# Kernel tuning notes

Hardware: AMD Instinct MI355X
Metric: run time of the kernel (lower is better)

Reference implementation:

```python
import jax, jax.numpy as jnp
import numpy as np

B, A, G, C, P, PH, PW = 8, 19248, 32, 81, 32, 138, 138
K_POS = 128            # fixed upper bound on positives used for the mask loss
INPUT_SIZE = 550.0
POS_THR, NEG_THR = 0.5, 0.4
ALPHA, GAMMA = 0.25, 2.0
NEG_POS_RATIO = 3
CLS_W, BOX_W, MASK_W = 1.0, 1.5, 6.125
VAR_XY, VAR_WH = 0.1, 0.2
EPS = 1e-6


def setup_inputs() -> dict:
    key = jax.random.key(0)
    ks = jax.random.split(key, 10)
    class_preds = jax.random.normal(ks[0], (B, A, C), jnp.float32)
    box_preds = jax.random.normal(ks[1], (B, A, 4), jnp.float32) * 0.1
    mask_coeffs = jax.random.normal(ks[2], (B, A, P), jnp.float32)
    prototypes = jax.random.normal(ks[3], (B, P, PH, PW), jnp.float32)
    # anchors in normalized [cx, cy, w, h]
    cxy = jax.random.uniform(ks[4], (A, 2), jnp.float32)
    wh = jax.random.uniform(ks[5], (A, 2), jnp.float32) * 0.25 + 0.02
    anchors = jnp.concatenate([cxy, wh], axis=-1)
    # GT boxes in absolute pixels [x1, y1, x2, y2] within 550x550
    xy1 = jax.random.uniform(ks[6], (B, G, 2), jnp.float32) * 380.0
    bwh = jax.random.uniform(ks[7], (B, G, 2), jnp.float32) * 150.0 + 15.0
    gt_boxes = jnp.concatenate([xy1, xy1 + bwh], axis=-1)
    gt_labels = jax.random.randint(ks[8], (B, G), 1, C)  # foreground classes
    gt_masks = (jax.random.uniform(ks[9], (B, G, PH, PW)) > 0.5).astype(jnp.float32)
    return {
        "class_preds": class_preds, "box_preds": box_preds,
        "mask_coeffs": mask_coeffs, "prototypes": prototypes,
        "anchors": anchors, "gt_boxes": gt_boxes,
        "gt_labels": gt_labels, "gt_masks": gt_masks,
    }


def _iou(a, b):
    # a: (A,4) xyxy, b: (G,4) xyxy -> (A,G)
    max_xy = jnp.minimum(a[:, None, 2:], b[None, :, 2:])
    min_xy = jnp.maximum(a[:, None, :2], b[None, :, :2])
    inter = jnp.clip(max_xy - min_xy, 0.0).prod(-1)
    area_a = (a[:, 2] - a[:, 0]) * (a[:, 3] - a[:, 1])
    area_b = (b[:, 2] - b[:, 0]) * (b[:, 3] - b[:, 1])
    union = area_a[:, None] + area_b[None, :] - inter
    return inter / jnp.clip(union, EPS)


def _smooth_l1(x):
    d = jnp.abs(x)
    return jnp.where(d < 1.0, 0.5 * d * d, d - 0.5)


def _image_loss(cls_p, box_p, coeffs, protos, gtb, gtl, gtm, anchors, anchors_xyxy):
    gtb = gtb / INPUT_SIZE                           # normalize to [0,1]
    iou = _iou(anchors_xyxy, gtb)                    # (A, G)
    best_gt_iou = iou.max(axis=1)                    # (A,)
    best_gt_idx = iou.argmax(axis=1)                 # (A,)
    best_anchor_idx = iou.argmax(axis=0)             # (G,) bipartite guarantee

    pos = best_gt_iou >= POS_THR
    pos = pos.at[best_anchor_idx].set(True)
    best_gt_idx = best_gt_idx.at[best_anchor_idx].set(jnp.arange(G))
    neg = (best_gt_iou < NEG_THR) & ~pos
    num_pos = pos.sum()
    # deterministic hard-negative cap at neg:pos = 3:1 (orig. uses randperm)
    neg = neg & (jnp.cumsum(neg) <= num_pos * NEG_POS_RATIO)

    matched_labels = jnp.where(pos, gtl[best_gt_idx], 0)   # 0 = background
    mb = gtb[best_gt_idx]                                  # (A,4) matched xyxy
    posf = pos.astype(jnp.float32)

    # ---- focal classification loss over pos|neg anchors ----
    probs = jax.nn.softmax(cls_p, axis=-1)
    p_t = jnp.take_along_axis(probs, matched_labels[:, None], axis=1)[:, 0]
    p_t = jnp.clip(p_t, EPS, 1.0 - EPS)
    alpha_t = jnp.where(matched_labels > 0, ALPHA, 1.0 - ALPHA)
    focal = alpha_t * (1.0 - p_t) ** GAMMA * (-jnp.log(p_t))
    cls_loss = (focal * (pos | neg).astype(jnp.float32)).sum()

    acx, acy, aw, ah = anchors[:, 0], anchors[:, 1], anchors[:, 2], anchors[:, 3]
    gcx = 0.5 * (mb[:, 0] + mb[:, 2]); gcy = 0.5 * (mb[:, 1] + mb[:, 3])
    gw = jnp.clip(mb[:, 2] - mb[:, 0], EPS); gh = jnp.clip(mb[:, 3] - mb[:, 1], EPS)
    t = jnp.stack([
        (gcx - acx) / (aw * VAR_XY),
        (gcy - acy) / (ah * VAR_XY),
        jnp.log(gw / aw) / VAR_WH,
        jnp.log(gh / ah) / VAR_WH,
    ], axis=-1)                                            # (A,4)
    box_loss = (_smooth_l1(box_p - t).sum(-1) * posf).sum()

    # ---- BCE mask loss on (up to K_POS) positive anchors ----
    score = jnp.where(pos, best_gt_iou + 1.0, 0.0)
    _, idx = jax.lax.top_k(score, K_POS)                   # (K,)
    w = posf[idx]                                          # 0-weight padding
    logits = jnp.einsum('kp,phw->khw', coeffs[idx], protos)  # (K,PH,PW)
    tgt = gtm[best_gt_idx[idx]]                            # (K,PH,PW)
    bce = jnp.maximum(logits, 0.0) - logits * tgt + jnp.log1p(jnp.exp(-jnp.abs(logits)))
    mask_loss = (bce.mean(axis=(1, 2)) * w).sum()

    return cls_loss, box_loss, mask_loss, num_pos


def reference(class_preds, box_preds, mask_coeffs, prototypes, anchors, gt_boxes, gt_labels, gt_masks):
    a_xyxy = jnp.concatenate(
        [anchors[:, :2] - anchors[:, 2:] * 0.5, anchors[:, :2] + anchors[:, 2:] * 0.5], axis=-1)
    cls_l, box_l, mask_l, npos = jax.vmap(
        _image_loss, in_axes=(0, 0, 0, 0, 0, 0, 0, None, None)
    )(class_preds, box_preds, mask_coeffs, prototypes, gt_boxes, gt_labels, gt_masks, anchors, a_xyxy)
    denom = jnp.maximum(npos.sum(), 1).astype(jnp.float32)
    total = (CLS_W * cls_l.sum() + BOX_W * box_l.sum() + MASK_W * mask_l.sum()) / denom
    return total
```

## Files before the change

### kernel.cpp

```cpp
#include <hip/hip_runtime.h>
#include <math.h>

#define BB 8
#define AA 19248
#define GG 32
#define CC 81
#define PP 32
#define PHW 19044
#define KPOS 128
#define NEGRATIO 3
#define SELCAP 7680
#define NWCH 304
#define NB1 76
#define NB0 75
#define NPT 1191
#define NB7 298
#define NB45 8

typedef _Float16 half8 __attribute__((ext_vector_type(8)));
typedef float floatx4 __attribute__((ext_vector_type(4)));

__device__ __forceinline__ float iou_one(float ax1, float ay1, float ax2, float ay2,
                                         float areaA,
                                         float gx1, float gy1, float gx2, float gy2) {
#pragma clang fp contract(off)
    float ix1 = fmaxf(ax1, gx1), iy1 = fmaxf(ay1, gy1);
    float ix2 = fminf(ax2, gx2), iy2 = fminf(ay2, gy2);
    float iw = fmaxf(ix2 - ix1, 0.0f), ih = fmaxf(iy2 - iy1, 0.0f);
    float inter = iw * ih;
    float areaB = (gx2 - gx1) * (gy2 - gy1);
    float u = areaA + areaB - inter;
    u = fmaxf(u, 1e-6f);
    return inter / u;
}

__global__ __launch_bounds__(256) void k01(
    const float* __restrict__ anchors, const float* __restrict__ gt_boxes,
    const float* __restrict__ protos, const float* __restrict__ gtm,
    float* __restrict__ best_iou, int* __restrict__ best_g,
    unsigned long long* __restrict__ gkey_part, float* __restrict__ acc,
    _Float16* __restrict__ protoT, unsigned* __restrict__ pmask) {
#pragma clang fp contract(off)
    int b = blockIdx.y;
    __shared__ float sg[GG][4];
    __shared__ unsigned long long s_gk[GG];

    if (blockIdx.x >= NB1) {
        int px = (blockIdx.x - NB1) * 256 + threadIdx.x;
        if (px >= PHW) return;
        const float* pb = protos + (size_t)b * PP * PHW + px;
        _Float16 v[PP];
        #pragma unroll
        for (int k = 0; k < PP; ++k)
            v[k] = (_Float16)pb[(size_t)k * PHW];
        half8* dst = (half8*)&protoT[((size_t)b * PHW + px) * PP];
        #pragma unroll
        for (int q = 0; q < 4; ++q)
            dst[q] = *(half8*)&v[q * 8];
        const float* gb = gtm + (size_t)b * GG * PHW + px;
        unsigned m = 0u;
        #pragma unroll
        for (int g = 0; g < GG; ++g)
            m |= (gb[(size_t)g * PHW] > 0.5f) ? (1u << g) : 0u;
        pmask[(size_t)b * PHW + px] = m;
        return;
    }

    int a = blockIdx.x * 256 + threadIdx.x;
    int lane = threadIdx.x & 63;
    if (blockIdx.x == 0 && b == 0 && threadIdx.x < 4)
        ((int*)acc)[threadIdx.x] = 0;
    for (int t = threadIdx.x; t < GG * 4; t += 256)
        sg[t >> 2][t & 3] = gt_boxes[b * GG * 4 + t] / 550.0f;
    if (threadIdx.x < GG) s_gk[threadIdx.x] = 0ULL;
    __syncthreads();
    bool valid = a < AA;
    int ac = valid ? a : AA - 1;
    float4 an = ((const float4*)anchors)[ac];
    float ax1 = an.x - an.z * 0.5f, ay1 = an.y - an.w * 0.5f;
    float ax2 = an.x + an.z * 0.5f, ay2 = an.y + an.w * 0.5f;
    float areaA = (ax2 - ax1) * (ay2 - ay1);
    unsigned long long bk = 0ULL;
    for (int gg = 0; gg < GG; ++gg) {
        int g = (gg + lane) & (GG - 1);
        float v = iou_one(ax1, ay1, ax2, ay2, areaA, sg[g][0], sg[g][1], sg[g][2], sg[g][3]);
        unsigned vb = __float_as_uint(v);
        unsigned long long k2 = ((unsigned long long)vb << 6) | (unsigned)(GG - 1 - g);
        if (k2 > bk) bk = k2;
        if (valid) {
            unsigned long long kg =
                ((unsigned long long)vb << 32) | (unsigned)(AA - 1 - a);
            atomicMax(&s_gk[g], kg);
        }
    }
    if (valid) {
        best_iou[b * AA + a] = __uint_as_float((unsigned)(bk >> 6));
        best_g[b * AA + a] = (GG - 1) - (int)(bk & 63ULL);
    }
    __syncthreads();
    if (threadIdx.x < GG)
        gkey_part[((size_t)b * NB1 + blockIdx.x) * GG + threadIdx.x] = s_gk[threadIdx.x];
}

__global__ __launch_bounds__(1024) void k3_match_scan(
    const float* __restrict__ best_iou, const int* __restrict__ best_g_in,
    const unsigned long long* __restrict__ gkey_part, const int* __restrict__ gtl,
    int* __restrict__ gidx_out, int* __restrict__ selmask,
    unsigned long long* __restrict__ pos_key,
    int* __restrict__ pos_cnt, int* __restrict__ g_npos,
    int* __restrict__ act_list, int* __restrict__ act_cnt) {
#pragma clang fp contract(off)
    int b = blockIdx.x;
    int tid = threadIdx.x;
    int lane = tid & 63, wid = tid >> 6;
    __shared__ short s_ov[AA];
    __shared__ unsigned long long s_gmax[GG];
    __shared__ int sba[GG];
    __shared__ int s_gtl[GG];
    __shared__ unsigned long long s_pmask[NWCH];
    __shared__ unsigned long long s_nmask[NWCH];
    __shared__ int s_woff[NWCH];
    __shared__ int s_wred[5];
    __shared__ int s_cnt, s_act;
    for (int i = tid; i < AA; i += 1024) s_ov[i] = -1;
    if (tid < GG) { s_gmax[tid] = 0ULL; s_gtl[tid] = gtl[b * GG + tid]; }
    if (tid == 0) { s_cnt = 0; s_act = 0; }
    __syncthreads();
    for (int c = tid >> 5; c < NB1; c += 32)
        atomicMax(&s_gmax[tid & 31],
                  gkey_part[((size_t)b * NB1 + c) * GG + (tid & 31)]);
    __syncthreads();
    if (tid < GG) sba[tid] = AA - 1 - (int)(unsigned)(s_gmax[tid] & 0xffffffffULL);
    __syncthreads();
    if (tid == 0) {
        for (int g = 0; g < GG; ++g) s_ov[sba[g]] = (short)g;
    }
    __syncthreads();

    for (int base = 0; base < AA; base += 1024) {
        int a = base + tid;
        bool p = false, npre = false;
        if (a < AA) {
            float biou = best_iou[b * AA + a];
            int ov = s_ov[a];
            int gi = (ov >= 0) ? ov : best_g_in[b * AA + a];
            p = (biou >= 0.5f) || (ov >= 0);
            npre = (biou < 0.4f) && !p;
            gidx_out[b * AA + a] = gi;
            selmask[b * AA + a] = p ? 2 : (npre ? 1 : 0);
            if (p) {
                int slot = atomicAdd(&s_cnt, 1);
                unsigned vb = __float_as_uint(biou + 1.0f);
                unsigned long long key =
                    ((unsigned long long)(vb - 0x3F800000u) << 32) |
                    (unsigned)(AA - 1 - a);
                pos_key[(size_t)b * AA + slot] = key;
            }
        }
        unsigned long long pm = __ballot(p);
        unsigned long long nm = __ballot(npre);
        if (lane == 0) {
            int w = (base >> 6) + wid;
            s_pmask[w] = pm;
            s_nmask[w] = nm;
        }
    }
    __syncthreads();
    int npos = s_cnt;
    if (tid == 0) { pos_cnt[b] = npos; atomicAdd(g_npos, npos); }
    int cap = npos * NEGRATIO;

    int c = (tid < NWCH) ? __popcll(s_nmask[tid]) : 0;
    int inc = c;
    if (wid < 5) {
        #pragma unroll
        for (int d = 1; d < 64; d <<= 1) {
            int t = __shfl_up(inc, d);
            if (lane >= d) inc += t;
        }
        if (lane == 63) s_wred[wid] = inc;
    }
    __syncthreads();
    if (tid == 0) {
        int run = 0;
        #pragma unroll
        for (int i = 0; i < 5; ++i) { int t = s_wred[i]; s_wred[i] = run; run += t; }
    }
    __syncthreads();
    if (tid < NWCH) s_woff[tid] = inc - c + s_wred[wid];
    __syncthreads();

    for (int base = 0; base < AA; base += 1024) {
        int a = base + tid;
        int w = (base >> 6) + wid;
        unsigned long long nm = s_nmask[w], pm = s_pmask[w];
        bool npre = (nm >> lane) & 1ULL;
        bool pos  = (pm >> lane) & 1ULL;
        int rank = __popcll(nm & ((1ULL << lane) - 1ULL));
        bool kept = npre && (s_woff[w] + rank + 1 <= cap);
        if (a < AA) {
            if (npre && !kept) selmask[b * AA + a] = 0;
            if (pos || kept) {
                int slot = atomicAdd(&s_act, 1);
                int gi = gidx_out[b * AA + a];
                int lbl = pos ? s_gtl[gi] : 0;
                unsigned e = (unsigned)a | ((unsigned)gi << 15) |
                             ((unsigned)lbl << 20) | (pos ? 0x80000000u : 0u);
                act_list[b * AA + slot] = (int)e;
            }
        }
    }
    __syncthreads();
    if (tid == 0) act_cnt[b] = s_act;
}

__global__ __launch_bounds__(1024) void k456(
    const float* __restrict__ cls_p, const int* __restrict__ act_list,
    const int* __restrict__ act_cnt, const float* __restrict__ box_p,
    const float* __restrict__ anchors, const float* __restrict__ gt_boxes,
    float* __restrict__ part_cls, float* __restrict__ part_box,
    const unsigned long long* __restrict__ pos_key, const int* __restrict__ pos_cnt,
    const int* __restrict__ gidx, const float* __restrict__ coeffs,
    int* __restrict__ sel_g, _Float16* __restrict__ sel_coef,
    int* __restrict__ sel_cnt) {
    int b = blockIdx.y;
    int tid = threadIdx.x;

    __shared__ unsigned long long s_keys[SELCAP];
    __shared__ int s_hist[256];
    __shared__ int s_sfx[256];
    __shared__ int s_wsum[4];
    __shared__ unsigned long long s_prefix;
    __shared__ int s_kk;
    __shared__ int s_nsel;
    __shared__ int s_sel_a[KPOS];
    __shared__ int s_sorted_a[KPOS];
    __shared__ int s_sorted_g[KPOS];
    __shared__ int s_gcnt[GG];
    __shared__ float s16a[16], s16b[16];

    if (blockIdx.x < NB45) {
        int n = act_cnt[b];
        float fsum = 0.0f, bsum = 0.0f;
        for (int i = blockIdx.x * 1024 + tid; i < n; i += NB45 * 1024) {
            unsigned e = (unsigned)act_list[b * AA + i];
            int a = e & 0x7fff;
            int g = (e >> 15) & 31;
            int lbl = (e >> 20) & 127;
            bool pos = (e >> 31) != 0u;
            const float* x = cls_p + (size_t)(b * AA + a) * CC;
            float v80 = x[80];
            float m0 = v80, m1 = -3.0e38f, m2 = -3.0e38f, m3 = -3.0e38f;
            #pragma unroll
            for (int q = 0; q < 20; ++q) {
                m0 = fmaxf(m0, x[4 * q + 0]); m1 = fmaxf(m1, x[4 * q + 1]);
                m2 = fmaxf(m2, x[4 * q + 2]); m3 = fmaxf(m3, x[4 * q + 3]);
            }
            float m = fmaxf(fmaxf(m0, m1), fmaxf(m2, m3));
            float s0 = __expf(v80 - m), s1 = 0.f, s2 = 0.f, s3 = 0.f;
            #pragma unroll
            for (int q = 0; q < 20; ++q) {
                s0 += __expf(x[4 * q + 0] - m); s1 += __expf(x[4 * q + 1] - m);
                s2 += __expf(x[4 * q + 2] - m); s3 += __expf(x[4 * q + 3] - m);
            }
            float s = (s0 + s1) + (s2 + s3);
            float pt = __expf(x[lbl] - m) / s;
            pt = fminf(fmaxf(pt, 1e-6f), 1.0f - 1e-6f);
            float at = (lbl > 0) ? 0.25f : 0.75f;
            float om = 1.0f - pt;
            fsum += at * om * om * (-__logf(pt));
            if (pos) {
#pragma clang fp contract(off)
                float4 mb = ((const float4*)gt_boxes)[b * GG + g];
                float4 an = ((const float4*)anchors)[a];
                const float4 bp = ((const float4*)box_p)[(size_t)b * AA + a];
                float q0 = mb.x / 550.0f, q1 = mb.y / 550.0f;
                float q2 = mb.z / 550.0f, q3 = mb.w / 550.0f;
                float gcx = 0.5f * (q0 + q2), gcy = 0.5f * (q1 + q3);
                float gw = fmaxf(q2 - q0, 1e-6f), gh = fmaxf(q3 - q1, 1e-6f);
                float t0 = (gcx - an.x) / (an.z * 0.1f);
                float t1 = (gcy - an.y) / (an.w * 0.1f);
                float t2 = logf(gw / an.z) / 0.2f;
                float t3 = logf(gh / an.w) / 0.2f;
                float d;
                d = fabsf(bp.x - t0); bsum += (d < 1.0f) ? 0.5f * d * d : d - 0.5f;
                d = fabsf(bp.y - t1); bsum += (d < 1.0f) ? 0.5f * d * d : d - 0.5f;
                d = fabsf(bp.z - t2); bsum += (d < 1.0f) ? 0.5f * d * d : d - 0.5f;
                d = fabsf(bp.w - t3); bsum += (d < 1.0f) ? 0.5f * d * d : d - 0.5f;
            }
        }
        for (int off = 32; off; off >>= 1) {
            fsum += __shfl_xor(fsum, off);
            bsum += __shfl_xor(bsum, off);
        }
        if ((tid & 63) == 0) { s16a[tid >> 6] = fsum; s16b[tid >> 6] = bsum; }
        __syncthreads();
        if (tid == 0) {
            float tf = 0.f, tb = 0.f;
            #pragma unroll
            for (int i = 0; i < 16; ++i) { tf += s16a[i]; tb += s16b[i]; }
            part_cls[b * NB45 + blockIdx.x] = tf;
            part_box[b * NB45 + blockIdx.x] = tb;
        }
        return;
    }

    int n = pos_cnt[b];
    int K = (n < KPOS) ? n : KPOS;
    const unsigned long long* keys;
    if (n <= SELCAP) {
        for (int i = tid; i < n; i += 1024) s_keys[i] = pos_key[(size_t)b * AA + i];
        keys = s_keys;
    } else {
        keys = pos_key + (size_t)b * AA;
    }
    if (tid == 0) { s_prefix = 0ULL; s_kk = KPOS; s_nsel = 0; }
    __syncthreads();

    if (n > KPOS) {
        for (int d = 6; d >= 0; --d) {
            unsigned long long pref = s_prefix;
            int kk = s_kk;
            int lane = tid & 63;
            if (tid < 256) s_hist[tid] = 0;
            __syncthreads();
            unsigned long long mhi = ~((1ULL << (8 * (d + 1))) - 1ULL);
            for (int i = tid; i < n; i += 1024) {
                unsigned long long k = keys[i];
                if ((k & mhi) == pref)
                    atomicAdd(&s_hist[(int)((k >> (8 * d)) & 255)], 1);
            }
            __syncthreads();
            int x = 0;
            if (tid < 256) {
                x = s_hist[255 - tid];
                #pragma unroll
                for (int o = 1; o < 64; o <<= 1) {
                    int t = __shfl_up(x, o);
                    if (lane >= o) x += t;
                }
                if (lane == 63) s_wsum[tid >> 6] = x;
            }
            __syncthreads();
            if (tid == 0) {
                int run = 0;
                #pragma unroll
                for (int i = 0; i < 4; ++i) { int t = s_wsum[i]; s_wsum[i] = run; run += t; }
            }
            __syncthreads();
            if (tid < 256) s_sfx[255 - tid] = x + s_wsum[tid >> 6];
            __syncthreads();
            if (tid < 256) {
                int v = tid;
                int ge = s_sfx[v];
                int gt = (v == 255) ? 0 : s_sfx[v + 1];
                if (ge >= kk && gt < kk) {
                    s_prefix = pref | ((unsigned long long)v << (8 * d));
                    s_kk = kk - gt;
                }
            }
            __syncthreads();
        }
    }

    unsigned long long T = (n > KPOS) ? s_prefix : 0ULL;
    for (int i = tid; i < n; i += 1024) {
        unsigned long long k = keys[i];
        if (k >= T) {
            int slot = atomicAdd(&s_nsel, 1);
            if (slot < KPOS)
                s_sel_a[slot] = AA - 1 - (int)(unsigned)(k & 0xffffffffu);
        }
    }
    __syncthreads();

    if (tid < GG) s_gcnt[tid] = 0;
    __syncthreads();
    int mya = -1, myg = -1;
    if (tid < K) {
        mya = s_sel_a[tid];
        myg = gidx[b * AA + mya];
        atomicAdd(&s_gcnt[myg], 1);
    }
    __syncthreads();
    if (tid == 0) {
        int run = 0;
        for (int g = 0; g < GG; ++g) { int c = s_gcnt[g]; s_gcnt[g] = run; run += c; }
    }
    __syncthreads();
    if (tid < K) {
        int pos = atomicAdd(&s_gcnt[myg], 1);
        s_sorted_a[pos] = mya;
        s_sorted_g[pos] = myg;
    }
    __syncthreads();

    if (tid == 0) sel_cnt[b] = K;
    int glast = (K > 0) ? s_sorted_g[K - 1] : 0;
    for (int t = tid; t < KPOS * PP; t += 1024) {
        int k = t >> 5, p = t & 31;
        _Float16 v = (_Float16)0.0f;
        if (k < K) {
            int a = s_sorted_a[k];
            v = (_Float16)coeffs[((size_t)(b * AA + a)) * PP + p];
        }
        sel_coef[(size_t)(b * KPOS + k) * PP + p] = v;
    }
    for (int t = tid; t < KPOS; t += 1024)
        sel_g[b * KPOS + t] = (t < K) ? s_sorted_g[t] : glast;
}

__global__ __launch_bounds__(256) void k7_mask(
    const _Float16* __restrict__ protoT, const unsigned* __restrict__ pmask,
    const _Float16* __restrict__ sel_coef, const int* __restrict__ sel_g,
    const int* __restrict__ sel_cnt, float* __restrict__ part_mask) {
    int b = blockIdx.y;
    int nk = sel_cnt[b];
    int tid = threadIdx.x;
    int wave = tid >> 6, lane = tid & 63;
    int lg = lane >> 4;
    int ln = lane & 15;
    int pt = blockIdx.x * 4 + wave;
    int px = pt * 16 + ln;
    bool pxv = (pt < NPT) && (px < PHW);
    int pc = pxv ? px : PHW - 1;

    half8 bfrag = *(const half8*)&protoT[((size_t)b * PHW + pc) * PP + lg * 8];
    unsigned gmask = pmask[(size_t)b * PHW + pc];

    const _Float16* ca = sel_coef + (size_t)b * KPOS * PP;
    const int* gb = sel_g + b * KPOS;

    half8 af[8];
    int4 gv[8];
    #pragma unroll
    for (int kt = 0; kt < 8; ++kt) {
        af[kt] = *(const half8*)&ca[(size_t)(kt * 16 + ln) * PP + lg * 8];
        gv[kt] = *(const int4*)&gb[kt * 16 + lg * 4];
    }

    float acc = 0.0f;
    #pragma unroll
    for (int kt = 0; kt < 8; ++kt) {
        floatx4 c = {0.f, 0.f, 0.f, 0.f};
        c = __builtin_amdgcn_mfma_f32_16x16x32_f16(af[kt], bfrag, c, 0, 0, 0);
        #pragma unroll
        for (int r = 0; r < 4; ++r) {
            int k = kt * 16 + lg * 4 + r;
            float l = c[r];
            int g0 = (r == 0) ? gv[kt].x : (r == 1) ? gv[kt].y
                   : (r == 2) ? gv[kt].z : gv[kt].w;
            float t = (float)((gmask >> g0) & 1u);
            float bce = fmaxf(l, 0.f) - l * t + __logf(1.f + __expf(-fabsf(l)));
            if (pxv && k < nk) acc += bce;
        }
    }

    for (int off = 32; off; off >>= 1) acc += __shfl_xor(acc, off);
    __shared__ float s_red[4];
    if (lane == 0) s_red[wave] = acc;
    __syncthreads();
    if (tid == 0)
        part_mask[(size_t)b * NB7 + blockIdx.x] =
            s_red[0] + s_red[1] + s_red[2] + s_red[3];
}

__global__ __launch_bounds__(1024) void k8_final(
    const float* __restrict__ part_cls, const float* __restrict__ part_box,
    const float* __restrict__ part_mask, const int* __restrict__ npos,
    float* __restrict__ out) {
    int tid = threadIdx.x;
    float c = 0.f, bx = 0.f, mk = 0.f;
    for (int i = tid; i < NB45 * BB; i += 1024) {
        c += part_cls[i];
        bx += part_box[i];
    }
    for (int i = tid; i < NB7 * BB; i += 1024)
        mk += part_mask[i];
    for (int off = 32; off; off >>= 1) {
        c += __shfl_xor(c, off);
        bx += __shfl_xor(bx, off);
        mk += __shfl_xor(mk, off);
    }
    __shared__ float sc[16], sb[16], sm[16];
    if ((tid & 63) == 0) {
        sc[tid >> 6] = c; sb[tid >> 6] = bx; sm[tid >> 6] = mk;
    }
    __syncthreads();
    if (tid == 0) {
        float tc = 0.f, tb = 0.f, tm = 0.f;
        #pragma unroll
        for (int i = 0; i < 16; ++i) { tc += sc[i]; tb += sb[i]; tm += sm[i]; }
        float denom = fmaxf((float)(*npos), 1.0f);
        out[0] = (1.0f * tc + 1.5f * tb + 6.125f * (tm / (float)PHW)) / denom;
    }
}

extern "C" void kernel_launch(void* const* d_in, const int* in_sizes, int n_in,
                              void* d_out, int out_size, void* d_ws, size_t ws_size,
                              hipStream_t stream) {
    (void)in_sizes; (void)n_in; (void)out_size; (void)ws_size;
    const float* class_preds = (const float*)d_in[0];
    const float* box_preds   = (const float*)d_in[1];
    const float* mask_coeffs = (const float*)d_in[2];
    const float* prototypes  = (const float*)d_in[3];
    const float* anchors     = (const float*)d_in[4];
    const float* gt_boxes    = (const float*)d_in[5];
    const int*   gt_labels   = (const int*)d_in[6];
    const float* gt_masks    = (const float*)d_in[7];
    float* out = (float*)d_out;

    size_t off = 0;
    char* w = (char*)d_ws;
    auto take = [&](size_t bytes) -> char* {
        char* p = w + off;
        off += (bytes + 255) & ~(size_t)255;
        return p;
    };
    float* acc      = (float*)take(32);
    float* best_iou = (float*)take((size_t)BB * AA * 4);
    int*   best_g   = (int*)  take((size_t)BB * AA * 4);
    int*   gidx     = (int*)  take((size_t)BB * AA * 4);
    int*   selmask  = (int*)  take((size_t)BB * AA * 4);
    unsigned long long* gkey_part =
        (unsigned long long*)take((size_t)BB * NB1 * GG * 8);
    int*   pos_cnt  = (int*)  take((size_t)BB * 4);
    unsigned long long* pos_key = (unsigned long long*)take((size_t)BB * AA * 8);
    int*   sel_g    = (int*)  take((size_t)BB * KPOS * 4);
    int*   sel_cnt  = (int*)  take((size_t)BB * 4);
    _Float16* sel_coef = (_Float16*)take((size_t)BB * KPOS * PP * 2);
    int*   act_list = (int*)  take((size_t)BB * AA * 4);
    int*   act_cnt  = (int*)  take((size_t)BB * 4);
    _Float16* protoT = (_Float16*)take((size_t)BB * PHW * PP * 2);
    unsigned* pmaskb = (unsigned*)take((size_t)BB * PHW * 4);
    float* part_cls  = (float*)take((size_t)BB * NB45 * 4);
    float* part_box  = (float*)take((size_t)BB * NB45 * 4);
    float* part_mask = (float*)take((size_t)BB * NB7 * 4);

    k01<<<dim3(NB1 + NB0, BB), 256, 0, stream>>>(
        anchors, gt_boxes, prototypes, gt_masks,
        best_iou, best_g, gkey_part, acc, protoT, pmaskb);
    k3_match_scan<<<BB, 1024, 0, stream>>>(
        best_iou, best_g, gkey_part, gt_labels, gidx, selmask, pos_key, pos_cnt,
        (int*)(acc + 3), act_list, act_cnt);
    k456<<<dim3(NB45 + 1, BB), 1024, 0, stream>>>(
        class_preds, act_list, act_cnt, box_preds, anchors, gt_boxes,
        part_cls, part_box,
        pos_key, pos_cnt, gidx, mask_coeffs, sel_g, sel_coef, sel_cnt);
    k7_mask<<<dim3(NB7, BB), 256, 0, stream>>>(
        protoT, pmaskb, sel_coef, sel_g, sel_cnt, part_mask);
    k8_final<<<1, 1024, 0, stream>>>(
        part_cls, part_box, part_mask, (int*)(acc + 3), out);
}
```

Baseline: 74.01 us.

## Move top-K positive selection into match-scan kernel and co-launch cls/box with mask loss

The radix-select of the top-K positives and the gathering of their coefficients move into the per-image match/scan kernel. Keys are cached in shared memory as they are produced, so they no longer have to be reloaded from global memory. The classification/box loss blocks and the mask-loss MFMA blocks now share one launch with 256-thread blocks, which removes a kernel launch and a dependency stage so the two independent workloads can overlap. The cost is that the single-block-per-image scan kernel carries more serial work and more shared memory (about 60KB of keys), which may lower its occupancy. The cls/box block count is also raised to fit the smaller blocks.

```diff
diff --git a/kernel.cpp b/kernel.cpp
--- a/kernel.cpp
+++ b/kernel.cpp
@@ -15,7 +15,7 @@
 #define NB0 75
 #define NPT 1191
 #define NB7 298
-#define NB45 8
+#define NB45 24
 
 typedef _Float16 half8 __attribute__((ext_vector_type(8)));
 typedef float floatx4 __attribute__((ext_vector_type(4)));
@@ -102,13 +102,16 @@
         gkey_part[((size_t)b * NB1 + blockIdx.x) * GG + threadIdx.x] = s_gk[threadIdx.x];
 }
 
-__global__ __launch_bounds__(1024) void k3_match_scan(
+__global__ __launch_bounds__(1024) void k36(
     const float* __restrict__ best_iou, const int* __restrict__ best_g_in,
     const unsigned long long* __restrict__ gkey_part, const int* __restrict__ gtl,
     int* __restrict__ gidx_out, int* __restrict__ selmask,
     unsigned long long* __restrict__ pos_key,
     int* __restrict__ pos_cnt, int* __restrict__ g_npos,
-    int* __restrict__ act_list, int* __restrict__ act_cnt) {
+    int* __restrict__ act_list, int* __restrict__ act_cnt,
+    const float* __restrict__ coeffs,
+    int* __restrict__ sel_g, _Float16* __restrict__ sel_coef,
+    int* __restrict__ sel_cnt) {
 #pragma clang fp contract(off)
     int b = blockIdx.x;
     int tid = threadIdx.x;
@@ -122,9 +125,21 @@
     __shared__ int s_woff[NWCH];
     __shared__ int s_wred[5];
     __shared__ int s_cnt, s_act;
+    __shared__ unsigned long long s_keys[SELCAP];
+    __shared__ int s_hist[256];
+    __shared__ int s_sfx[256];
+    __shared__ int s_wsum[4];
+    __shared__ unsigned long long s_prefix;
+    __shared__ int s_kk;
+    __shared__ int s_nsel;
+    __shared__ int s_sel_a[KPOS];
+    __shared__ int s_sorted_a[KPOS];
+    __shared__ int s_sorted_g[KPOS];
+    __shared__ int s_gcnt[GG];
+
     for (int i = tid; i < AA; i += 1024) s_ov[i] = -1;
     if (tid < GG) { s_gmax[tid] = 0ULL; s_gtl[tid] = gtl[b * GG + tid]; }
-    if (tid == 0) { s_cnt = 0; s_act = 0; }
+    if (tid == 0) { s_cnt = 0; s_act = 0; s_prefix = 0ULL; s_kk = KPOS; s_nsel = 0; }
     __syncthreads();
     for (int c = tid >> 5; c < NB1; c += 32)
         atomicMax(&s_gmax[tid & 31],
@@ -155,6 +170,7 @@
                     ((unsigned long long)(vb - 0x3F800000u) << 32) |
                     (unsigned)(AA - 1 - a);
                 pos_key[(size_t)b * AA + slot] = key;
+                if (slot < SELCAP) s_keys[slot] = key;
             }
         }
         unsigned long long pm = __ballot(p);
@@ -212,37 +228,120 @@
     }
     __syncthreads();
     if (tid == 0) act_cnt[b] = s_act;
+
+    int n = npos;
+    int K = (n < KPOS) ? n : KPOS;
+    const unsigned long long* keys =
+        (n <= SELCAP) ? s_keys : (pos_key + (size_t)b * AA);
+    __syncthreads();
+
+    if (n > KPOS) {
+        for (int d = 6; d >= 0; --d) {
+            unsigned long long pref = s_prefix;
+            int kk = s_kk;
+            if (tid < 256) s_hist[tid] = 0;
+            __syncthreads();
+            unsigned long long mhi = ~((1ULL << (8 * (d + 1))) - 1ULL);
+            for (int i = tid; i < n; i += 1024) {
+                unsigned long long k = keys[i];
+                if ((k & mhi) == pref)
+                    atomicAdd(&s_hist[(int)((k >> (8 * d)) & 255)], 1);
+            }
+            __syncthreads();
+            int x = 0;
+            if (tid < 256) {
+                x = s_hist[255 - tid];
+                #pragma unroll
+                for (int o = 1; o < 64; o <<= 1) {
+                    int t = __shfl_up(x, o);
+                    if (lane >= o) x += t;
+                }
+                if (lane == 63) s_wsum[tid >> 6] = x;
+            }
+            __syncthreads();
+            if (tid == 0) {
+                int run = 0;
+                #pragma unroll
+                for (int i = 0; i < 4; ++i) { int t = s_wsum[i]; s_wsum[i] = run; run += t; }
+            }
+            __syncthreads();
+            if (tid < 256) s_sfx[255 - tid] = x + s_wsum[tid >> 6];
+            __syncthreads();
+            if (tid < 256) {
+                int v = tid;
+                int ge = s_sfx[v];
+                int gt = (v == 255) ? 0 : s_sfx[v + 1];
+                if (ge >= kk && gt < kk) {
+                    s_prefix = pref | ((unsigned long long)v << (8 * d));
+                    s_kk = kk - gt;
+                }
+            }
+            __syncthreads();
+        }
+    }
+
+    unsigned long long T = (n > KPOS) ? s_prefix : 0ULL;
+    for (int i = tid; i < n; i += 1024) {
+        unsigned long long k = keys[i];
+        if (k >= T) {
+            int slot = atomicAdd(&s_nsel, 1);
+            if (slot < KPOS)
+                s_sel_a[slot] = AA - 1 - (int)(unsigned)(k & 0xffffffffu);
+        }
+    }
+    __syncthreads();
+
+    if (tid < GG) s_gcnt[tid] = 0;
+    __syncthreads();
+    int mya = -1, myg = -1;
+    if (tid < K) {
+        mya = s_sel_a[tid];
+        myg = gidx_out[b * AA + mya];
+        atomicAdd(&s_gcnt[myg], 1);
+    }
+    __syncthreads();
+    if (tid == 0) {
+        int run = 0;
+        for (int g = 0; g < GG; ++g) { int cg = s_gcnt[g]; s_gcnt[g] = run; run += cg; }
+    }
+    __syncthreads();
+    if (tid < K) {
+        int pos = atomicAdd(&s_gcnt[myg], 1);
+        s_sorted_a[pos] = mya;
+        s_sorted_g[pos] = myg;
+    }
+    __syncthreads();
+
+    if (tid == 0) sel_cnt[b] = K;
+    int glast = (K > 0) ? s_sorted_g[K - 1] : 0;
+    for (int t = tid; t < KPOS * PP; t += 1024) {
+        int k = t >> 5, p = t & 31;
+        _Float16 v = (_Float16)0.0f;
+        if (k < K) {
+            int a = s_sorted_a[k];
+            v = (_Float16)coeffs[((size_t)(b * AA + a)) * PP + p];
+        }
+        sel_coef[(size_t)(b * KPOS + k) * PP + p] = v;
+    }
+    for (int t = tid; t < KPOS; t += 1024)
+        sel_g[b * KPOS + t] = (t < K) ? s_sorted_g[t] : glast;
 }
 
-__global__ __launch_bounds__(1024) void k456(
+__global__ __launch_bounds__(256) void k457(
     const float* __restrict__ cls_p, const int* __restrict__ act_list,
     const int* __restrict__ act_cnt, const float* __restrict__ box_p,
     const float* __restrict__ anchors, const float* __restrict__ gt_boxes,
     float* __restrict__ part_cls, float* __restrict__ part_box,
-    const unsigned long long* __restrict__ pos_key, const int* __restrict__ pos_cnt,
-    const int* __restrict__ gidx, const float* __restrict__ coeffs,
-    int* __restrict__ sel_g, _Float16* __restrict__ sel_coef,
-    int* __restrict__ sel_cnt) {
+    const _Float16* __restrict__ protoT, const unsigned* __restrict__ pmask,
+    const _Float16* __restrict__ sel_coef, const int* __restrict__ sel_g,
+    const int* __restrict__ sel_cnt, float* __restrict__ part_mask) {
     int b = blockIdx.y;
     int tid = threadIdx.x;
-
-    __shared__ unsigned long long s_keys[SELCAP];
-    __shared__ int s_hist[256];
-    __shared__ int s_sfx[256];
-    __shared__ int s_wsum[4];
-    __shared__ unsigned long long s_prefix;
-    __shared__ int s_kk;
-    __shared__ int s_nsel;
-    __shared__ int s_sel_a[KPOS];
-    __shared__ int s_sorted_a[KPOS];
-    __shared__ int s_sorted_g[KPOS];
-    __shared__ int s_gcnt[GG];
-    __shared__ float s16a[16], s16b[16];
 
     if (blockIdx.x < NB45) {
         int n = act_cnt[b];
         float fsum = 0.0f, bsum = 0.0f;
-        for (int i = blockIdx.x * 1024 + tid; i < n; i += NB45 * 1024) {
+        for (int i = blockIdx.x * 256 + tid; i < n; i += NB45 * 256) {
             unsigned e = (unsigned)act_list[b * AA + i];
             int a = e & 0x7fff;
             int g = (e >> 15) & 31;
@@ -293,134 +392,21 @@
             fsum += __shfl_xor(fsum, off);
             bsum += __shfl_xor(bsum, off);
         }
-        if ((tid & 63) == 0) { s16a[tid >> 6] = fsum; s16b[tid >> 6] = bsum; }
+        __shared__ float s4f[4], s4b[4];
+        if ((tid & 63) == 0) { s4f[tid >> 6] = fsum; s4b[tid >> 6] = bsum; }
         __syncthreads();
         if (tid == 0) {
-            float tf = 0.f, tb = 0.f;
-            #pragma unroll
-            for (int i = 0; i < 16; ++i) { tf += s16a[i]; tb += s16b[i]; }
-            part_cls[b * NB45 + blockIdx.x] = tf;
-            part_box[b * NB45 + blockIdx.x] = tb;
+            part_cls[b * NB45 + blockIdx.x] = s4f[0] + s4f[1] + s4f[2] + s4f[3];
+            part_box[b * NB45 + blockIdx.x] = s4b[0] + s4b[1] + s4b[2] + s4b[3];
         }
         return;
     }
 
-    int n = pos_cnt[b];
-    int K = (n < KPOS) ? n : KPOS;
-    const unsigned long long* keys;
-    if (n <= SELCAP) {
-        for (int i = tid; i < n; i += 1024) s_keys[i] = pos_key[(size_t)b * AA + i];
-        keys = s_keys;
-    } else {
-        keys = pos_key + (size_t)b * AA;
-    }
-    if (tid == 0) { s_prefix = 0ULL; s_kk = KPOS; s_nsel = 0; }
-    __syncthreads();
-
-    if (n > KPOS) {
-        for (int d = 6; d >= 0; --d) {
-            unsigned long long pref = s_prefix;
-            int kk = s_kk;
-            int lane = tid & 63;
-            if (tid < 256) s_hist[tid] = 0;
-            __syncthreads();
-            unsigned long long mhi = ~((1ULL << (8 * (d + 1))) - 1ULL);
-            for (int i = tid; i < n; i += 1024) {
-                unsigned long long k = keys[i];
-                if ((k & mhi) == pref)
-                    atomicAdd(&s_hist[(int)((k >> (8 * d)) & 255)], 1);
-            }
-            __syncthreads();
-            int x = 0;
-            if (tid < 256) {
-                x = s_hist[255 - tid];
-                #pragma unroll
-                for (int o = 1; o < 64; o <<= 1) {
-                    int t = __shfl_up(x, o);
-                    if (lane >= o) x += t;
-                }
-                if (lane == 63) s_wsum[tid >> 6] = x;
-            }
-            __syncthreads();
-            if (tid == 0) {
-                int run = 0;
-                #pragma unroll
-                for (int i = 0; i < 4; ++i) { int t = s_wsum[i]; s_wsum[i] = run; run += t; }
-            }
-            __syncthreads();
-            if (tid < 256) s_sfx[255 - tid] = x + s_wsum[tid >> 6];
-            __syncthreads();
-            if (tid < 256) {
-                int v = tid;
-                int ge = s_sfx[v];
-                int gt = (v == 255) ? 0 : s_sfx[v + 1];
-                if (ge >= kk && gt < kk) {
-                    s_prefix = pref | ((unsigned long long)v << (8 * d));
-                    s_kk = kk - gt;
-                }
-            }
-            __syncthreads();
-        }
-    }
-
-    unsigned long long T = (n > KPOS) ? s_prefix : 0ULL;
-    for (int i = tid; i < n; i += 1024) {
-        unsigned long long k = keys[i];
-        if (k >= T) {
-            int slot = atomicAdd(&s_nsel, 1);
-            if (slot < KPOS)
-                s_sel_a[slot] = AA - 1 - (int)(unsigned)(k & 0xffffffffu);
-        }
-    }
-    __syncthreads();
-
-    if (tid < GG) s_gcnt[tid] = 0;
-    __syncthreads();
-    int mya = -1, myg = -1;
-    if (tid < K) {
-        mya = s_sel_a[tid];
-        myg = gidx[b * AA + mya];
-        atomicAdd(&s_gcnt[myg], 1);
-    }
-    __syncthreads();
-    if (tid == 0) {
-        int run = 0;
-        for (int g = 0; g < GG; ++g) { int c = s_gcnt[g]; s_gcnt[g] = run; run += c; }
-    }
-    __syncthreads();
-    if (tid < K) {
-        int pos = atomicAdd(&s_gcnt[myg], 1);
-        s_sorted_a[pos] = mya;
-        s_sorted_g[pos] = myg;
-    }
-    __syncthreads();
-
-    if (tid == 0) sel_cnt[b] = K;
-    int glast = (K > 0) ? s_sorted_g[K - 1] : 0;
-    for (int t = tid; t < KPOS * PP; t += 1024) {
-        int k = t >> 5, p = t & 31;
-        _Float16 v = (_Float16)0.0f;
-        if (k < K) {
-            int a = s_sorted_a[k];
-            v = (_Float16)coeffs[((size_t)(b * AA + a)) * PP + p];
-        }
-        sel_coef[(size_t)(b * KPOS + k) * PP + p] = v;
-    }
-    for (int t = tid; t < KPOS; t += 1024)
-        sel_g[b * KPOS + t] = (t < K) ? s_sorted_g[t] : glast;
-}
-
-__global__ __launch_bounds__(256) void k7_mask(
-    const _Float16* __restrict__ protoT, const unsigned* __restrict__ pmask,
-    const _Float16* __restrict__ sel_coef, const int* __restrict__ sel_g,
-    const int* __restrict__ sel_cnt, float* __restrict__ part_mask) {
-    int b = blockIdx.y;
     int nk = sel_cnt[b];
-    int tid = threadIdx.x;
     int wave = tid >> 6, lane = tid & 63;
     int lg = lane >> 4;
     int ln = lane & 15;
-    int pt = blockIdx.x * 4 + wave;
+    int pt = (blockIdx.x - NB45) * 4 + wave;
     int px = pt * 16 + ln;
     bool pxv = (pt < NPT) && (px < PHW);
     int pc = pxv ? px : PHW - 1;
@@ -461,7 +447,7 @@
     if (lane == 0) s_red[wave] = acc;
     __syncthreads();
     if (tid == 0)
-        part_mask[(size_t)b * NB7 + blockIdx.x] =
+        part_mask[(size_t)b * NB7 + (blockIdx.x - NB45)] =
             s_red[0] + s_red[1] + s_red[2] + s_red[3];
 }
 
@@ -540,14 +526,13 @@
     k01<<<dim3(NB1 + NB0, BB), 256, 0, stream>>>(
         anchors, gt_boxes, prototypes, gt_masks,
         best_iou, best_g, gkey_part, acc, protoT, pmaskb);
-    k3_match_scan<<<BB, 1024, 0, stream>>>(
+    k36<<<BB, 1024, 0, stream>>>(
         best_iou, best_g, gkey_part, gt_labels, gidx, selmask, pos_key, pos_cnt,
-        (int*)(acc + 3), act_list, act_cnt);
-    k456<<<dim3(NB45 + 1, BB), 1024, 0, stream>>>(
+        (int*)(acc + 3), act_list, act_cnt,
+        mask_coeffs, sel_g, sel_coef, sel_cnt);
+    k457<<<dim3(NB45 + NB7, BB), 256, 0, stream>>>(
         class_preds, act_list, act_cnt, box_preds, anchors, gt_boxes,
         part_cls, part_box,
-        pos_key, pos_cnt, gidx, mask_coeffs, sel_g, sel_coef, sel_cnt);
-    k7_mask<<<dim3(NB7, BB), 256, 0, stream>>>(
         protoT, pmaskb, sel_coef, sel_g, sel_cnt, part_mask);
     k8_final<<<1, 1024, 0, stream>>>(
         part_cls, part_box, part_mask, (int*)(acc + 3), out);
```

Measured after the change: 71.96 us. 1.03x faster.
